# Kernel optimization log

Hardware: AMD Instinct MI355X
Metric: run time of the kernel (lower is better)

## Reference

```python
import jax, jax.numpy as jnp
import numpy as np
from jax import lax

B, HIST, FC, N, F = 64, 24, 24, 1000, 8
EMB, HID, NEMB, OUT = 32, 64, 1000, 1
IN = EMB + OUT  # GRU input dim


def setup_inputs() -> dict:
    key = jax.random.key(0)
    ks = jax.random.split(key, 11)
    X = jax.random.normal(ks[0], (B, HIST + FC, N, F), jnp.float32)
    idx = jax.random.randint(ks[1], (B, HIST + FC, N), 0, NEMB)
    X = X.at[..., -1].set(idx.astype(jnp.float32))  # last channel = spatial ids
    hn = jax.random.normal(ks[2], (B * N, HID), jnp.float32)
    xn = jax.random.normal(ks[3], (B, N, OUT), jnp.float32)
    s = 0.1
    emb_table = jax.random.normal(ks[4], (NEMB, EMB), jnp.float32) * s
    W_ih = jax.random.normal(ks[5], (3 * HID, IN), jnp.float32) * s
    W_hh = jax.random.normal(ks[6], (3 * HID, HID), jnp.float32) * s
    b_ih = jax.random.normal(ks[7], (3 * HID,), jnp.float32) * s
    b_hh = jax.random.normal(ks[8], (3 * HID,), jnp.float32) * s
    W_out = jax.random.normal(ks[9], (OUT, HID), jnp.float32) * s
    b_out = jax.random.normal(ks[10], (OUT,), jnp.float32) * s
    return {"X": X, "hn": hn, "xn": xn, "emb_table": emb_table,
            "W_ih": W_ih, "W_hh": W_hh, "b_ih": b_ih, "b_hh": b_hh,
            "W_out": W_out, "b_out": b_out}


def reference(X, hn, xn, emb_table, W_ih, W_hh, b_ih, b_hh, W_out, b_out):
    # indices for the forecast steps: [FC, B, N]
    idx_seq = X[:, :FC, :, -1].astype(jnp.int32).transpose(1, 0, 2)

    def step(carry, idx_t):
        h, x_prev = carry                      # h: [B*N, HID], x_prev: [B, N, 1]
        emb = emb_table[idx_t]                 # [B, N, EMB] gather
        x = jnp.concatenate([x_prev, emb], axis=-1).reshape(B * N, IN)
        gi = x @ W_ih.T + b_ih                 # [B*N, 3*HID]
        gh = h @ W_hh.T + b_hh
        i_r, i_z, i_n = jnp.split(gi, 3, axis=-1)
        h_r, h_z, h_n = jnp.split(gh, 3, axis=-1)
        r = jax.nn.sigmoid(i_r + h_r)
        z = jax.nn.sigmoid(i_z + h_z)
        n = jnp.tanh(i_n + r * h_n)
        h_new = (1.0 - z) * n + z * h
        out = h_new.reshape(B, N, HID) @ W_out.T + b_out  # [B, N, 1]
        return (h_new, out), out

    _, preds = lax.scan(step, (hn, xn), idx_seq)  # preds: [FC, B, N, 1]
    return preds.transpose(1, 0, 2, 3)            # [B, FC, N, 1]
```

## Files before the change

### kernel.cpp

```cpp
#include <hip/hip_runtime.h>
#include <math.h>

#define BB   64
#define FC   24
#define NN   1000
#define HID  64
#define EMBD 32
#define TT   48
#define FF   8
#define NEMB 1000
#define G3   192
#define INSZ 33

#define CPB  32
#define TPB  256
#define MT   2
#define AST  72

#define EPB  8

typedef __attribute__((ext_vector_type(8))) short bf16x8;
typedef __attribute__((ext_vector_type(4))) float f32x4;

static __device__ __forceinline__ unsigned short f2bf(float f) {
    unsigned u = __builtin_bit_cast(unsigned, f);
    u += 0x7FFFu + ((u >> 16) & 1u);
    return (unsigned short)(u >> 16);
}
static __device__ __forceinline__ float fast_sigmoid(float v) {
    float e = __builtin_amdgcn_exp2f(-1.4426950408889634f * v);
    return __builtin_amdgcn_rcpf(1.0f + e);
}
static __device__ __forceinline__ float fast_tanh(float v) {
    float vv = fminf(fmaxf(v, -15.0f), 15.0f);
    float e = __builtin_amdgcn_exp2f(2.8853900817779268f * vv);
    return 1.0f - 2.0f * __builtin_amdgcn_rcpf(e + 1.0f);
}

__global__ __launch_bounds__(256) void premul_kernel(
    const float* __restrict__ emb, const float* __restrict__ Wih,
    const float* __restrict__ bih, const float* __restrict__ bhh,
    float* __restrict__ P3)
{
    __shared__ float Wihs[INSZ * G3];
    __shared__ float xes[EPB * EMBD];
    const int tid = threadIdx.x;
    const int e0  = blockIdx.x * EPB;

    for (int i = tid; i < G3 * INSZ; i += 256) {
        int j = i / INSZ, k = i - j * INSZ;
        Wihs[k * G3 + j] = Wih[i];
    }
    xes[tid] = emb[(size_t)e0 * EMBD + tid];
    __syncthreads();

    const int el = tid >> 5;
    const float* xe = xes + el * EMBD;
    #pragma unroll
    for (int i = 0; i < G3 / 32; ++i) {
        int j = (tid & 31) + 32 * i;
        float acc = bih[j] + (j < 2 * HID ? bhh[j] : 0.0f);
        #pragma unroll
        for (int k = 0; k < EMBD; ++k)
            acc = fmaf(Wihs[(k + 1) * G3 + j], xe[k], acc);
        P3[(size_t)(e0 + el) * G3 + (j & 63) * 3 + (j >> 6)] = acc;
    }
}

__global__ __launch_bounds__(TPB) __attribute__((amdgpu_waves_per_eu(4)))
void gru_decoder(
    const float* __restrict__ X,
    const float* __restrict__ hn0,
    const float* __restrict__ xn,
    const float* __restrict__ Whh,
    const float* __restrict__ bhh,
    const float* __restrict__ Wih,
    const float* __restrict__ Wout,
    const float* __restrict__ bout,
    const float* __restrict__ P3,
    float* __restrict__ out)
{
    __shared__ __align__(16) unsigned short Abuf[CPB * AST];
    __shared__ int   idxbuf[FC * CPB];
    __shared__ float xbuf[CPB];

    const int tid  = threadIdx.x;
    const int lane = tid & 63;
    const int g    = tid >> 6;
    const int quad = lane >> 4;
    const int l15  = lane & 15;
    const int jcol = g * 16 + l15;
    const int rowb = quad * 4;
    const int cell0 = blockIdx.x * CPB;

    for (int e = tid; e < FC * CPB; e += TPB) {
        int t = e >> 5, m = e & 31;
        int cell = cell0 + m;
        int b = cell / NN, n = cell - b * NN;
        idxbuf[t * CPB + m] = (int)X[(((size_t)b * TT + t) * NN + n) * FF + 7];
    }
    if (tid < CPB) xbuf[tid] = xn[cell0 + tid];

    bf16x8 Bf[3][2];
    #pragma unroll
    for (int gate = 0; gate < 3; ++gate) {
        #pragma unroll
        for (int ks = 0; ks < 2; ++ks) {
            const float* src = Whh + (size_t)(gate * HID + jcol) * HID + ks * 32 + quad * 8;
            float4 lo = *(const float4*)src;
            float4 hi = *(const float4*)(src + 4);
            bf16x8 f;
            f[0] = (short)f2bf(lo.x); f[1] = (short)f2bf(lo.y);
            f[2] = (short)f2bf(lo.z); f[3] = (short)f2bf(lo.w);
            f[4] = (short)f2bf(hi.x); f[5] = (short)f2bf(hi.y);
            f[6] = (short)f2bf(hi.z); f[7] = (short)f2bf(hi.w);
            Bf[gate][ks] = f;
        }
    }

    const float w0r = Wih[(size_t)jcol * INSZ];
    const float w0z = Wih[(size_t)(HID + jcol) * INSZ];
    const float w0n = Wih[(size_t)(2 * HID + jcol) * INSZ];
    const float bhn = bhh[2 * HID + jcol];
    const float bout0 = bout[0];

    const int cd_m   = g * 8 + (lane & 7);
    const int kslice = lane >> 3;
    float wout_r[8];
    #pragma unroll
    for (int e2 = 0; e2 < 8; ++e2) wout_r[e2] = Wout[kslice * 8 + e2];
    const int cd_cell = cell0 + cd_m;
    const int cd_b = cd_cell / NN, cd_n = cd_cell - cd_b * NN;
    const size_t obase = (size_t)cd_b * FC * NN + cd_n;

    float hold[MT][4];
    #pragma unroll
    for (int mt = 0; mt < MT; ++mt) {
        #pragma unroll
        for (int rr = 0; rr < 4; ++rr) {
            int m = mt * 16 + rowb + rr;
            float h = hn0[((size_t)cell0 + m) * HID + jcol];
            hold[mt][rr] = h;
            Abuf[m * AST + jcol] = f2bf(h);
        }
    }
    __syncthreads();

    for (int t = 0; t < FC; ++t) {
        f32x4 accr[MT], accz[MT], accn[MT];
        #pragma unroll
        for (int mt = 0; mt < MT; ++mt) {
            const bf16x8 a0 = *(const bf16x8*)&Abuf[(mt * 16 + l15) * AST + quad * 8];
            const bf16x8 a1 = *(const bf16x8*)&Abuf[(mt * 16 + l15) * AST + 32 + quad * 8];
            f32x4 z4 = {0.f, 0.f, 0.f, 0.f};
            accr[mt] = __builtin_amdgcn_mfma_f32_16x16x32_bf16(a0, Bf[0][0], z4, 0, 0, 0);
            accr[mt] = __builtin_amdgcn_mfma_f32_16x16x32_bf16(a1, Bf[0][1], accr[mt], 0, 0, 0);
            accz[mt] = __builtin_amdgcn_mfma_f32_16x16x32_bf16(a0, Bf[1][0], z4, 0, 0, 0);
            accz[mt] = __builtin_amdgcn_mfma_f32_16x16x32_bf16(a1, Bf[1][1], accz[mt], 0, 0, 0);
            accn[mt] = __builtin_amdgcn_mfma_f32_16x16x32_bf16(a0, Bf[2][0], z4, 0, 0, 0);
            accn[mt] = __builtin_amdgcn_mfma_f32_16x16x32_bf16(a1, Bf[2][1], accn[mt], 0, 0, 0);
        }

        if (t > 0) {
            bf16x8 hv = *(const bf16x8*)&Abuf[cd_m * AST + kslice * 8];
            const unsigned* hv32 = (const unsigned*)&hv;
            float o = 0.f;
            #pragma unroll
            for (int q = 0; q < 4; ++q) {
                unsigned v = hv32[q];
                o = fmaf(wout_r[2 * q],     __builtin_bit_cast(float, v << 16),         o);
                o = fmaf(wout_r[2 * q + 1], __builtin_bit_cast(float, v & 0xFFFF0000u), o);
            }
            o += __shfl_xor(o, 8);
            o += __shfl_xor(o, 16);
            o += __shfl_xor(o, 32);
            if (lane < 8) {
                float oo = o + bout0;
                out[obase + (size_t)(t - 1) * NN] = oo;
                xbuf[cd_m] = oo;
            }
        }
        __syncthreads();

        #pragma unroll
        for (int mt = 0; mt < MT; ++mt) {
            #pragma unroll
            for (int rr = 0; rr < 4; ++rr) {
                int m   = mt * 16 + rowb + rr;
                int idx = idxbuf[t * CPB + m];
                float xp = xbuf[m];
                const float* pp = P3 + (size_t)idx * G3 + jcol * 3;
                float ar = fmaf(w0r, xp, pp[0]);
                float az = fmaf(w0z, xp, pp[1]);
                float an = fmaf(w0n, xp, pp[2]);
                float r  = fast_sigmoid(ar + accr[mt][rr]);
                float z  = fast_sigmoid(az + accz[mt][rr]);
                float nv = fast_tanh(an + r * (accn[mt][rr] + bhn));
                float hnew = nv + z * (hold[mt][rr] - nv);
                hold[mt][rr] = hnew;
                Abuf[m * AST + jcol] = f2bf(hnew);
            }
        }
        __syncthreads();
    }

    {
        bf16x8 hv = *(const bf16x8*)&Abuf[cd_m * AST + kslice * 8];
        const unsigned* hv32 = (const unsigned*)&hv;
        float o = 0.f;
        #pragma unroll
        for (int q = 0; q < 4; ++q) {
            unsigned v = hv32[q];
            o = fmaf(wout_r[2 * q],     __builtin_bit_cast(float, v << 16),         o);
            o = fmaf(wout_r[2 * q + 1], __builtin_bit_cast(float, v & 0xFFFF0000u), o);
        }
        o += __shfl_xor(o, 8);
        o += __shfl_xor(o, 16);
        o += __shfl_xor(o, 32);
        if (lane < 8) out[obase + (size_t)(FC - 1) * NN] = o + bout0;
    }
}

extern "C" void kernel_launch(void* const* d_in, const int* in_sizes, int n_in,
                              void* d_out, int out_size, void* d_ws, size_t ws_size,
                              hipStream_t stream) {
    (void)in_sizes; (void)n_in; (void)out_size; (void)ws_size;
    const float* X    = (const float*)d_in[0];
    const float* hn   = (const float*)d_in[1];
    const float* xn   = (const float*)d_in[2];
    const float* emb  = (const float*)d_in[3];
    const float* Wih  = (const float*)d_in[4];
    const float* Whh  = (const float*)d_in[5];
    const float* bih  = (const float*)d_in[6];
    const float* bhh  = (const float*)d_in[7];
    const float* Wout = (const float*)d_in[8];
    const float* bout = (const float*)d_in[9];
    float* out = (float*)d_out;
    float* P3  = (float*)d_ws;

    premul_kernel<<<NEMB / EPB, 256, 0, stream>>>(emb, Wih, bih, bhh, P3);

    const int blocks = (BB * NN) / CPB;
    gru_decoder<<<blocks, TPB, 0, stream>>>(X, hn, xn, Whh, bhh, Wih,
                                            Wout, bout, P3, out);
}
```

Baseline: 266.6 us.

## Fuse embedding input projection into GRU kernel via MFMA with prefetched bf16 embeddings

Removes the separate premultiply kernel that built a per-embedding gate table in global memory. The decoder now gathers raw embedding rows each step, converts them to bf16 into a double-buffered shared tile one step ahead, and computes the input projection with extra MFMA instructions, folding biases into the accumulator init. Gate writes are packed with a hardware bf16 pair convert. This drops a kernel launch and the scattered per-element P3 loads in the gate loop, at the cost of more MFMA work per step and bf16 rounding of the embedding and W_ih.

Result: slower. 544.5 us (+104.2%).

```diff
diff --git a/kernel.cpp b/kernel.cpp
--- a/kernel.cpp
+++ b/kernel.cpp
@@ -16,8 +16,7 @@
 #define TPB  256
 #define MT   2
 #define AST  72
-
-#define EPB  8
+#define XST  32
 
 typedef __attribute__((ext_vector_type(8))) short bf16x8;
 typedef __attribute__((ext_vector_type(4))) float f32x4;
@@ -27,6 +26,11 @@
     u += 0x7FFFu + ((u >> 16) & 1u);
     return (unsigned short)(u >> 16);
 }
+static __device__ __forceinline__ unsigned cvt_pk_bf16(float a, float b) {
+    unsigned r;
+    asm("v_cvt_pk_bf16_f32 %0, %1, %2" : "=v"(r) : "v"(a), "v"(b));
+    return r;
+}
 static __device__ __forceinline__ float fast_sigmoid(float v) {
     float e = __builtin_amdgcn_exp2f(-1.4426950408889634f * v);
     return __builtin_amdgcn_rcpf(1.0f + e);
@@ -35,36 +39,6 @@
     float vv = fminf(fmaxf(v, -15.0f), 15.0f);
     float e = __builtin_amdgcn_exp2f(2.8853900817779268f * vv);
     return 1.0f - 2.0f * __builtin_amdgcn_rcpf(e + 1.0f);
-}
-
-__global__ __launch_bounds__(256) void premul_kernel(
-    const float* __restrict__ emb, const float* __restrict__ Wih,
-    const float* __restrict__ bih, const float* __restrict__ bhh,
-    float* __restrict__ P3)
-{
-    __shared__ float Wihs[INSZ * G3];
-    __shared__ float xes[EPB * EMBD];
-    const int tid = threadIdx.x;
-    const int e0  = blockIdx.x * EPB;
-
-    for (int i = tid; i < G3 * INSZ; i += 256) {
-        int j = i / INSZ, k = i - j * INSZ;
-        Wihs[k * G3 + j] = Wih[i];
-    }
-    xes[tid] = emb[(size_t)e0 * EMBD + tid];
-    __syncthreads();
-
-    const int el = tid >> 5;
-    const float* xe = xes + el * EMBD;
-    #pragma unroll
-    for (int i = 0; i < G3 / 32; ++i) {
-        int j = (tid & 31) + 32 * i;
-        float acc = bih[j] + (j < 2 * HID ? bhh[j] : 0.0f);
-        #pragma unroll
-        for (int k = 0; k < EMBD; ++k)
-            acc = fmaf(Wihs[(k + 1) * G3 + j], xe[k], acc);
-        P3[(size_t)(e0 + el) * G3 + (j & 63) * 3 + (j >> 6)] = acc;
-    }
 }
 
 __global__ __launch_bounds__(TPB) __attribute__((amdgpu_waves_per_eu(4)))
@@ -72,15 +46,17 @@
     const float* __restrict__ X,
     const float* __restrict__ hn0,
     const float* __restrict__ xn,
+    const float* __restrict__ emb,
+    const float* __restrict__ Wih,
     const float* __restrict__ Whh,
+    const float* __restrict__ bih,
     const float* __restrict__ bhh,
-    const float* __restrict__ Wih,
     const float* __restrict__ Wout,
     const float* __restrict__ bout,
-    const float* __restrict__ P3,
     float* __restrict__ out)
 {
     __shared__ __align__(16) unsigned short Abuf[CPB * AST];
+    __shared__ __align__(16) unsigned short Xt[2][CPB * XST];
     __shared__ int   idxbuf[FC * CPB];
     __shared__ float xbuf[CPB];
 
@@ -117,10 +93,22 @@
             Bf[gate][ks] = f;
         }
     }
+    bf16x8 BX[3];
+    #pragma unroll
+    for (int gate = 0; gate < 3; ++gate) {
+        const float* src = Wih + (size_t)(gate * HID + jcol) * INSZ + 1 + quad * 8;
+        bf16x8 f;
+        #pragma unroll
+        for (int e = 0; e < 8; ++e) f[e] = (short)f2bf(src[e]);
+        BX[gate] = f;
+    }
 
     const float w0r = Wih[(size_t)jcol * INSZ];
     const float w0z = Wih[(size_t)(HID + jcol) * INSZ];
     const float w0n = Wih[(size_t)(2 * HID + jcol) * INSZ];
+    const float br  = bih[jcol] + bhh[jcol];
+    const float bz  = bih[HID + jcol] + bhh[HID + jcol];
+    const float bni = bih[2 * HID + jcol];
     const float bhn = bhh[2 * HID + jcol];
     const float bout0 = bout[0];
 
@@ -146,19 +134,46 @@
     }
     __syncthreads();
 
+    {
+        int r8 = tid >> 3, k4 = (tid & 7) * 4;
+        int idx = idxbuf[r8];
+        float4 e4 = *(const float4*)(emb + (size_t)idx * EMBD + k4);
+        unsigned p0 = cvt_pk_bf16(e4.x, e4.y);
+        unsigned p1 = cvt_pk_bf16(e4.z, e4.w);
+        *(uint2*)&Xt[0][r8 * XST + k4] = make_uint2(p0, p1);
+    }
+    __syncthreads();
+
     for (int t = 0; t < FC; ++t) {
-        f32x4 accr[MT], accz[MT], accn[MT];
+        if (t + 1 < FC) {
+            int r8 = tid >> 3, k4 = (tid & 7) * 4;
+            int idx = idxbuf[(t + 1) * CPB + r8];
+            float4 e4 = *(const float4*)(emb + (size_t)idx * EMBD + k4);
+            unsigned p0 = cvt_pk_bf16(e4.x, e4.y);
+            unsigned p1 = cvt_pk_bf16(e4.z, e4.w);
+            *(uint2*)&Xt[(t + 1) & 1][r8 * XST + k4] = make_uint2(p0, p1);
+        }
+        const unsigned short* Xc = Xt[t & 1];
+
+        f32x4 accr[MT], accz[MT], accni[MT], accng[MT];
         #pragma unroll
         for (int mt = 0; mt < MT; ++mt) {
             const bf16x8 a0 = *(const bf16x8*)&Abuf[(mt * 16 + l15) * AST + quad * 8];
             const bf16x8 a1 = *(const bf16x8*)&Abuf[(mt * 16 + l15) * AST + 32 + quad * 8];
-            f32x4 z4 = {0.f, 0.f, 0.f, 0.f};
-            accr[mt] = __builtin_amdgcn_mfma_f32_16x16x32_bf16(a0, Bf[0][0], z4, 0, 0, 0);
-            accr[mt] = __builtin_amdgcn_mfma_f32_16x16x32_bf16(a1, Bf[0][1], accr[mt], 0, 0, 0);
-            accz[mt] = __builtin_amdgcn_mfma_f32_16x16x32_bf16(a0, Bf[1][0], z4, 0, 0, 0);
-            accz[mt] = __builtin_amdgcn_mfma_f32_16x16x32_bf16(a1, Bf[1][1], accz[mt], 0, 0, 0);
-            accn[mt] = __builtin_amdgcn_mfma_f32_16x16x32_bf16(a0, Bf[2][0], z4, 0, 0, 0);
-            accn[mt] = __builtin_amdgcn_mfma_f32_16x16x32_bf16(a1, Bf[2][1], accn[mt], 0, 0, 0);
+            const bf16x8 x0 = *(const bf16x8*)&Xc[(mt * 16 + l15) * XST + quad * 8];
+            f32x4 cr  = {br,  br,  br,  br };
+            f32x4 cz  = {bz,  bz,  bz,  bz };
+            f32x4 cni = {bni, bni, bni, bni};
+            f32x4 cng = {bhn, bhn, bhn, bhn};
+            accr[mt]  = __builtin_amdgcn_mfma_f32_16x16x32_bf16(x0, BX[0], cr, 0, 0, 0);
+            accr[mt]  = __builtin_amdgcn_mfma_f32_16x16x32_bf16(a0, Bf[0][0], accr[mt], 0, 0, 0);
+            accr[mt]  = __builtin_amdgcn_mfma_f32_16x16x32_bf16(a1, Bf[0][1], accr[mt], 0, 0, 0);
+            accz[mt]  = __builtin_amdgcn_mfma_f32_16x16x32_bf16(x0, BX[1], cz, 0, 0, 0);
+            accz[mt]  = __builtin_amdgcn_mfma_f32_16x16x32_bf16(a0, Bf[1][0], accz[mt], 0, 0, 0);
+            accz[mt]  = __builtin_amdgcn_mfma_f32_16x16x32_bf16(a1, Bf[1][1], accz[mt], 0, 0, 0);
+            accni[mt] = __builtin_amdgcn_mfma_f32_16x16x32_bf16(x0, BX[2], cni, 0, 0, 0);
+            accng[mt] = __builtin_amdgcn_mfma_f32_16x16x32_bf16(a0, Bf[2][0], cng, 0, 0, 0);
+            accng[mt] = __builtin_amdgcn_mfma_f32_16x16x32_bf16(a1, Bf[2][1], accng[mt], 0, 0, 0);
         }
 
         if (t > 0) {
@@ -185,20 +200,25 @@
         #pragma unroll
         for (int mt = 0; mt < MT; ++mt) {
             #pragma unroll
-            for (int rr = 0; rr < 4; ++rr) {
-                int m   = mt * 16 + rowb + rr;
-                int idx = idxbuf[t * CPB + m];
-                float xp = xbuf[m];
-                const float* pp = P3 + (size_t)idx * G3 + jcol * 3;
-                float ar = fmaf(w0r, xp, pp[0]);
-                float az = fmaf(w0z, xp, pp[1]);
-                float an = fmaf(w0n, xp, pp[2]);
-                float r  = fast_sigmoid(ar + accr[mt][rr]);
-                float z  = fast_sigmoid(az + accz[mt][rr]);
-                float nv = fast_tanh(an + r * (accn[mt][rr] + bhn));
-                float hnew = nv + z * (hold[mt][rr] - nv);
-                hold[mt][rr] = hnew;
-                Abuf[m * AST + jcol] = f2bf(hnew);
+            for (int rp = 0; rp < 2; ++rp) {
+                float h2[2];
+                #pragma unroll
+                for (int k = 0; k < 2; ++k) {
+                    const int rr = rp * 2 + k;
+                    const int m  = mt * 16 + rowb + rr;
+                    float xp = xbuf[m];
+                    float r  = fast_sigmoid(fmaf(w0r, xp, accr[mt][rr]));
+                    float z  = fast_sigmoid(fmaf(w0z, xp, accz[mt][rr]));
+                    float nv = fast_tanh(fmaf(r, accng[mt][rr],
+                                              fmaf(w0n, xp, accni[mt][rr])));
+                    float hnew = nv + z * (hold[mt][rr] - nv);
+                    hold[mt][rr] = hnew;
+                    h2[k] = hnew;
+                }
+                unsigned pk = cvt_pk_bf16(h2[0], h2[1]);
+                const int m0 = mt * 16 + rowb + rp * 2;
+                Abuf[m0 * AST + jcol]       = (unsigned short)pk;
+                Abuf[(m0 + 1) * AST + jcol] = (unsigned short)(pk >> 16);
             }
         }
         __syncthreads();
@@ -224,7 +244,7 @@
 extern "C" void kernel_launch(void* const* d_in, const int* in_sizes, int n_in,
                               void* d_out, int out_size, void* d_ws, size_t ws_size,
                               hipStream_t stream) {
-    (void)in_sizes; (void)n_in; (void)out_size; (void)ws_size;
+    (void)in_sizes; (void)n_in; (void)out_size; (void)d_ws; (void)ws_size;
     const float* X    = (const float*)d_in[0];
     const float* hn   = (const float*)d_in[1];
     const float* xn   = (const float*)d_in[2];
@@ -236,11 +256,8 @@
     const float* Wout = (const float*)d_in[8];
     const float* bout = (const float*)d_in[9];
     float* out = (float*)d_out;
-    float* P3  = (float*)d_ws;
-
-    premul_kernel<<<NEMB / EPB, 256, 0, stream>>>(emb, Wih, bih, bhh, P3);
 
     const int blocks = (BB * NN) / CPB;
-    gru_decoder<<<blocks, TPB, 0, stream>>>(X, hn, xn, Whh, bhh, Wih,
-                                            Wout, bout, P3, out);
-}
+    gru_decoder<<<blocks, TPB, 0, stream>>>(X, hn, xn, emb, Wih, Whh,
+                                            bih, bhh, Wout, bout, out);
+}
```
